# Optimization experiments

Hardware: AMD Instinct MI355X
Metric: run time of the kernel (lower is better)

## Reference

```python
import jax, jax.numpy as jnp
import numpy as np

G = 0.001
EPS = 1e-6


def setup_inputs() -> dict:
    key = jax.random.key(0)
    k1, k2 = jax.random.split(key)
    B, N, D = 8, 4096, 3
    q = jax.random.normal(k1, (B, N, D), dtype=jnp.float32)
    m = jax.random.uniform(k2, (N,), dtype=jnp.float32)
    return {"q": q, "m": m}


def reference(q, m):
    # q: (B, N, D), m: (N,)
    N = q.shape[-2]
    diff = q[:, :, None, :] - q[:, None, :, :]          # (B, N, N, D)
    dist = jnp.sqrt(jnp.sum(diff * diff, axis=-1) + EPS)  # (B, N, N)
    mass_matrix = m[:, None] * m[None, :]                # (N, N)
    V = -G * mass_matrix / dist                          # (B, N, N)
    # zero the diagonal (self-interaction), matching fill_(0.0)
    off_diag = 1.0 - jnp.eye(N, dtype=q.dtype)
    V = V * off_diag
    return jnp.sum(V, axis=(-1, -2)) / 2.0               # (B,)
```

## Files before the change

kernel.cpp:

```cpp
#include <hip/hip_runtime.h>

typedef float v2f __attribute__((ext_vector_type(2)));
typedef float v4f __attribute__((ext_vector_type(4)));

#define BLK 256
#define IPT 8
#define TI (BLK * IPT)
#define TJ 64
#define G_CONST 0.001f
#define EPS_CONST 1e-6f

__global__ __launch_bounds__(BLK, 4)
void grav_kernel(const float* __restrict__ q, const float* __restrict__ m,
                 float* __restrict__ out, int N) {
  const int b   = blockIdx.z;
  const int tid = threadIdx.x;
  const int j0  = blockIdx.y * TJ;
  const int i0  = blockIdx.x * TI;

  __shared__ float xs[TJ], ys[TJ], zs[TJ], ms[TJ];
  __shared__ float wsum[4];

  const float* qb = q + (size_t)b * N * 3;

  if (tid < TJ) {
    const int j = j0 + tid;
    xs[tid] = qb[3 * j + 0];
    ys[tid] = qb[3 * j + 1];
    zs[tid] = qb[3 * j + 2];
    ms[tid] = m[j];
  }

  v2f xi2[IPT], yi2[IPT], zi2[IPT];
  float mi[IPT];
#pragma unroll
  for (int s = 0; s < IPT; ++s) {
    const int i = i0 + s * BLK + tid;
    const float x = qb[3 * i + 0];
    const float y = qb[3 * i + 1];
    const float z = qb[3 * i + 2];
    xi2[s] = (v2f){x, x};
    yi2[s] = (v2f){y, y};
    zi2[s] = (v2f){z, z};
    mi[s]  = m[i];
  }

  __syncthreads();

  const v2f eps2 = {EPS_CONST, EPS_CONST};
  v2f acc[IPT] = {};

  for (int k = 0; k < TJ; k += 4) {
    const v4f jx = *(const v4f*)&xs[k];
    const v4f jy = *(const v4f*)&ys[k];
    const v4f jz = *(const v4f*)&zs[k];
    const v4f jm = *(const v4f*)&ms[k];
    const v2f jx0 = {jx.x, jx.y}, jx1 = {jx.z, jx.w};
    const v2f jy0 = {jy.x, jy.y}, jy1 = {jy.z, jy.w};
    const v2f jz0 = {jz.x, jz.y}, jz1 = {jz.z, jz.w};
    const v2f jm0 = {jm.x, jm.y}, jm1 = {jm.z, jm.w};

#pragma unroll
    for (int s = 0; s < IPT; ++s) {
      const v2f dx0 = jx0 - xi2[s], dy0 = jy0 - yi2[s], dz0 = jz0 - zi2[s];
      const v2f dx1 = jx1 - xi2[s], dy1 = jy1 - yi2[s], dz1 = jz1 - zi2[s];

      v2f r0 = __builtin_elementwise_fma(dz0, dz0, eps2);
      v2f r1 = __builtin_elementwise_fma(dz1, dz1, eps2);
      r0 = __builtin_elementwise_fma(dy0, dy0, r0);
      r1 = __builtin_elementwise_fma(dy1, dy1, r1);
      r0 = __builtin_elementwise_fma(dx0, dx0, r0);
      r1 = __builtin_elementwise_fma(dx1, dx1, r1);

      const v2f ri0 = {__builtin_amdgcn_rsqf(r0.x), __builtin_amdgcn_rsqf(r0.y)};
      const v2f ri1 = {__builtin_amdgcn_rsqf(r1.x), __builtin_amdgcn_rsqf(r1.y)};

      acc[s] = __builtin_elementwise_fma(jm0, ri0, acc[s]);
      acc[s] = __builtin_elementwise_fma(jm1, ri1, acc[s]);
    }
  }

  float tsum = 0.f;
#pragma unroll
  for (int s = 0; s < IPT; ++s) {
    const int i = i0 + s * BLK + tid;
    float h = acc[s].x + acc[s].y;
    if (i >= j0 && i < j0 + TJ) h -= mi[s] * __builtin_amdgcn_rsqf(EPS_CONST);
    tsum += mi[s] * h;
  }

#pragma unroll
  for (int off = 32; off > 0; off >>= 1) tsum += __shfl_down(tsum, off);
  const int wid  = tid >> 6;
  const int lane = tid & 63;
  if (lane == 0) wsum[wid] = tsum;
  __syncthreads();
  if (tid == 0) {
    const float s = (wsum[0] + wsum[1]) + (wsum[2] + wsum[3]);
    atomicAdd(out + b, s * (-0.5f * G_CONST));
  }
}

extern "C" void kernel_launch(void* const* d_in, const int* in_sizes, int n_in,
                              void* d_out, int out_size, void* d_ws, size_t ws_size,
                              hipStream_t stream) {
  const float* q = (const float*)d_in[0];
  const float* m = (const float*)d_in[1];
  float* out = (float*)d_out;

  const int N = in_sizes[1];
  const int B = in_sizes[0] / (N * 3);

  hipMemsetAsync(out, 0, (size_t)out_size * sizeof(float), stream);

  dim3 grid(N / TI, N / TJ, B);
  grav_kernel<<<grid, BLK, 0, stream>>>(q, m, out, N);
}
```

Baseline: 35.19 us.

## Halve rows per thread, raise occupancy, and software-prefetch shared j-tiles

```diff
diff --git a/kernel.cpp b/kernel.cpp
--- a/kernel.cpp
+++ b/kernel.cpp
@@ -4,13 +4,13 @@
 typedef float v4f __attribute__((ext_vector_type(4)));
 
 #define BLK 256
-#define IPT 8
+#define IPT 4
 #define TI (BLK * IPT)
 #define TJ 64
 #define G_CONST 0.001f
 #define EPS_CONST 1e-6f
 
-__global__ __launch_bounds__(BLK, 4)
+__global__ __launch_bounds__(BLK, 6)
 void grav_kernel(const float* __restrict__ q, const float* __restrict__ m,
                  float* __restrict__ out, int N) {
   const int b   = blockIdx.z;
@@ -31,18 +31,14 @@
     ms[tid] = m[j];
   }
 
-  v2f xi2[IPT], yi2[IPT], zi2[IPT];
-  float mi[IPT];
+  float xi[IPT], yi[IPT], zi[IPT], mi[IPT];
 #pragma unroll
   for (int s = 0; s < IPT; ++s) {
     const int i = i0 + s * BLK + tid;
-    const float x = qb[3 * i + 0];
-    const float y = qb[3 * i + 1];
-    const float z = qb[3 * i + 2];
-    xi2[s] = (v2f){x, x};
-    yi2[s] = (v2f){y, y};
-    zi2[s] = (v2f){z, z};
-    mi[s]  = m[i];
+    xi[s] = qb[3 * i + 0];
+    yi[s] = qb[3 * i + 1];
+    zi[s] = qb[3 * i + 2];
+    mi[s] = m[i];
   }
 
   __syncthreads();
@@ -50,11 +46,18 @@
   const v2f eps2 = {EPS_CONST, EPS_CONST};
   v2f acc[IPT] = {};
 
+  v4f jx = *(const v4f*)&xs[0];
+  v4f jy = *(const v4f*)&ys[0];
+  v4f jz = *(const v4f*)&zs[0];
+  v4f jm = *(const v4f*)&ms[0];
+
   for (int k = 0; k < TJ; k += 4) {
-    const v4f jx = *(const v4f*)&xs[k];
-    const v4f jy = *(const v4f*)&ys[k];
-    const v4f jz = *(const v4f*)&zs[k];
-    const v4f jm = *(const v4f*)&ms[k];
+    const int kn = (k + 4) & (TJ - 1);
+    const v4f nx = *(const v4f*)&xs[kn];
+    const v4f ny = *(const v4f*)&ys[kn];
+    const v4f nz = *(const v4f*)&zs[kn];
+    const v4f nm = *(const v4f*)&ms[kn];
+
     const v2f jx0 = {jx.x, jx.y}, jx1 = {jx.z, jx.w};
     const v2f jy0 = {jy.x, jy.y}, jy1 = {jy.z, jy.w};
     const v2f jz0 = {jz.x, jz.y}, jz1 = {jz.z, jz.w};
@@ -62,8 +65,9 @@
 
 #pragma unroll
     for (int s = 0; s < IPT; ++s) {
-      const v2f dx0 = jx0 - xi2[s], dy0 = jy0 - yi2[s], dz0 = jz0 - zi2[s];
-      const v2f dx1 = jx1 - xi2[s], dy1 = jy1 - yi2[s], dz1 = jz1 - zi2[s];
+      const v2f xi2 = {xi[s], xi[s]}, yi2 = {yi[s], yi[s]}, zi2 = {zi[s], zi[s]};
+      const v2f dx0 = jx0 - xi2, dy0 = jy0 - yi2, dz0 = jz0 - zi2;
+      const v2f dx1 = jx1 - xi2, dy1 = jy1 - yi2, dz1 = jz1 - zi2;
 
       v2f r0 = __builtin_elementwise_fma(dz0, dz0, eps2);
       v2f r1 = __builtin_elementwise_fma(dz1, dz1, eps2);
@@ -78,6 +82,8 @@
       acc[s] = __builtin_elementwise_fma(jm0, ri0, acc[s]);
       acc[s] = __builtin_elementwise_fma(jm1, ri1, acc[s]);
     }
+
+    jx = nx; jy = ny; jz = nz; jm = nm;
   }
 
   float tsum = 0.f;
```

New measurement: 41.41 us. +17.7%, slower.
